# Optimization experiments

Measured on AMD Instinct MI355X. Metric: run time of the kernel, lower is better.

The kernel has to match this reference:

```python
import jax, jax.numpy as jnp
import numpy as np
import math

NUM_HEADS = 16


def rotate_half(x):
    # faithful to torch: take even/odd interleaved halves, cat(-x2, x1)
    x1 = x[..., ::2]
    x2 = x[..., 1::2]
    return jnp.concatenate((-x2, x1), axis=-1)


def rotary_tables(seq_len, head_dim, dtype):
    inv_freq = 1.0 / (10000.0 ** (jnp.arange(0, head_dim, 2, dtype=jnp.float32) / head_dim))
    t = jnp.arange(seq_len, dtype=jnp.float32)
    freqs = t[:, None] * inv_freq[None, :]           # [T, hd/2]
    emb = jnp.concatenate((freqs, freqs), axis=-1)   # [T, hd]
    cos = jnp.cos(emb)[None, None, :, :].astype(dtype)
    sin = jnp.sin(emb)[None, None, :, :].astype(dtype)
    return cos, sin


def setup_inputs() -> dict:
    key = jax.random.key(0)
    k1, k2, k3, k4 = jax.random.split(key, 4)
    B, T, D = 2, 2048, 1024
    scale = 1.0 / math.sqrt(D)
    x = jax.random.normal(k1, (B, T, D), dtype=jnp.float32)
    w_qkv = jax.random.normal(k2, (3 * D, D), dtype=jnp.float32) * scale
    w_out = jax.random.normal(k3, (D, D), dtype=jnp.float32) * scale
    b_out = jax.random.normal(k4, (D,), dtype=jnp.float32) * scale
    return {"x": x, "w_qkv": w_qkv, "w_out": w_out, "b_out": b_out}


def reference(x, w_qkv, w_out, b_out):
    B, T, D = x.shape
    H = NUM_HEADS
    hd = D // H

    qkv = x @ w_qkv.T                                # [B, T, 3D]
    q, k, v = jnp.split(qkv, 3, axis=-1)
    def to_heads(a):
        return a.reshape(B, T, H, hd).transpose(0, 2, 1, 3)  # [B, H, T, hd]
    q, k, v = to_heads(q), to_heads(k), to_heads(v)

    cos, sin = rotary_tables(T, hd, x.dtype)
    q = q * cos + rotate_half(q) * sin
    k = k * cos + rotate_half(k) * sin

    attn = jnp.einsum("bhqd,bhkd->bhqk", q, k) / math.sqrt(hd)
    attn = jax.nn.softmax(attn, axis=-1)
    out = jnp.einsum("bhqk,bhkd->bhqd", attn, v)
    out = out.transpose(0, 2, 1, 3).reshape(B, T, D)
    return out @ w_out.T + b_out
```

## Files before the change

kernel.cpp:

```cpp
#include <hip/hip_runtime.h>
#include <math.h>

#define B_ 2
#define T_ 2048
#define D_ 1024
#define H_ 16

typedef __attribute__((ext_vector_type(8))) short bf16x8;
typedef __attribute__((ext_vector_type(4))) float f32x4;
typedef __attribute__((address_space(3))) char lds_char;
typedef __attribute__((address_space(1))) const char g_char;

#define QSCALE 0.18033688011112042f
#define DEFER_THR 11.5f

static __device__ inline unsigned short bf16_rne(float f) {
    union { float f; unsigned u; } v; v.f = f;
    unsigned r = v.u + 0x7FFFu + ((v.u >> 16) & 1u);
    return (unsigned short)(r >> 16);
}
static __device__ inline unsigned pack2bf(float lo, float hi) {
    return (unsigned)bf16_rne(lo) | ((unsigned)bf16_rne(hi) << 16);
}

__global__ __launch_bounds__(256) void split_kernel(const float* __restrict__ in,
                                                    unsigned short* __restrict__ hi,
                                                    unsigned short* __restrict__ lo,
                                                    int n8) {
    int i = blockIdx.x * 256 + threadIdx.x;
    if (i >= n8) return;
    const float4* ip = (const float4*)in + (size_t)i * 2;
    float4 f0 = ip[0], f1 = ip[1];
    float fs[8] = {f0.x, f0.y, f0.z, f0.w, f1.x, f1.y, f1.z, f1.w};
    unsigned hu[4], lu[4];
#pragma unroll
    for (int j = 0; j < 4; ++j) {
        unsigned short h0 = bf16_rne(fs[2 * j]), h1 = bf16_rne(fs[2 * j + 1]);
        union { unsigned u; float f; } c0, c1;
        c0.u = (unsigned)h0 << 16; c1.u = (unsigned)h1 << 16;
        unsigned short l0 = bf16_rne(fs[2 * j] - c0.f);
        unsigned short l1 = bf16_rne(fs[2 * j + 1] - c1.f);
        hu[j] = (unsigned)h0 | ((unsigned)h1 << 16);
        lu[j] = (unsigned)l0 | ((unsigned)l1 << 16);
    }
    *(uint4*)(hi + (size_t)i * 8) = make_uint4(hu[0], hu[1], hu[2], hu[3]);
    *(uint4*)(lo + (size_t)i * 8) = make_uint4(lu[0], lu[1], lu[2], lu[3]);
}

__global__ __launch_bounds__(256) void rope_tables(float* __restrict__ cosT,
                                                   float* __restrict__ sinT) {
    int idx = blockIdx.x * 256 + threadIdx.x;
    int t = idx >> 5, i = idx & 31;
    double invf_d = exp(-((double)(2 * i) / 64.0) * 9.210340371976184);
    float invf = (float)invf_d;
    float ang = (float)t * invf;
    cosT[idx] = (float)cos((double)ang);
    sinT[idx] = (float)sin((double)ang);
}

template <int BIAS>
__global__ __launch_bounds__(256) void gemm_split(const unsigned short* __restrict__ Ahi,
                                                  const unsigned short* __restrict__ Alo,
                                                  const unsigned short* __restrict__ Bhi,
                                                  const unsigned short* __restrict__ Blo,
                                                  const float* __restrict__ bias,
                                                  float* __restrict__ C,
                                                  int M, int N, int K) {
    __shared__ alignas(16) char lds[32768];
    char* As_hi = lds;
    char* As_lo = lds + 8192;
    char* Bs_hi = lds + 16384;
    char* Bs_lo = lds + 24576;

    const int tid = threadIdx.x, l = tid & 63, w = tid >> 6;
    const int m0 = blockIdx.y * 128, n0 = blockIdx.x * 128;
    const int wr = (w >> 1) * 64, wc = (w & 1) * 64;
    const int q16 = l & 15, g8 = l >> 4;
    const int srow = w * 16 + (l >> 2);

    f32x4 acc[4][4];
#pragma unroll
    for (int i = 0; i < 4; ++i)
#pragma unroll
        for (int j = 0; j < 4; ++j) acc[i][j] = (f32x4){0.f, 0.f, 0.f, 0.f};

    for (int k0 = 0; k0 < K; k0 += 32) {
#pragma unroll
        for (int rd = 0; rd < 2; ++rd) {
            int row = srow + rd * 64;
            int g = (l & 3) ^ (row & 3);
            size_t goffA = (size_t)(m0 + row) * K + k0 + g * 8;
            size_t goffB = (size_t)(n0 + row) * K + k0 + g * 8;
            int lbase = rd * 4096 + w * 1024;
            __builtin_amdgcn_global_load_lds((g_char*)(Ahi + goffA), (lds_char*)(As_hi + lbase), 16, 0, 0);
            __builtin_amdgcn_global_load_lds((g_char*)(Alo + goffA), (lds_char*)(As_lo + lbase), 16, 0, 0);
            __builtin_amdgcn_global_load_lds((g_char*)(Bhi + goffB), (lds_char*)(Bs_hi + lbase), 16, 0, 0);
            __builtin_amdgcn_global_load_lds((g_char*)(Blo + goffB), (lds_char*)(Bs_lo + lbase), 16, 0, 0);
        }
        __syncthreads();

        bf16x8 ah[4], al[4], bh[4], bl[4];
#pragma unroll
        for (int i = 0; i < 4; ++i) {
            int ra = wr + 16 * i + q16, rb = wc + 16 * i + q16;
            ah[i] = *(const bf16x8*)(As_hi + ra * 64 + ((g8 ^ (ra & 3)) * 16));
            al[i] = *(const bf16x8*)(As_lo + ra * 64 + ((g8 ^ (ra & 3)) * 16));
            bh[i] = *(const bf16x8*)(Bs_hi + rb * 64 + ((g8 ^ (rb & 3)) * 16));
            bl[i] = *(const bf16x8*)(Bs_lo + rb * 64 + ((g8 ^ (rb & 3)) * 16));
        }
#pragma unroll
        for (int i = 0; i < 4; ++i)
#pragma unroll
            for (int j = 0; j < 4; ++j) {
                acc[i][j] = __builtin_amdgcn_mfma_f32_16x16x32_bf16(ah[i], bh[j], acc[i][j], 0, 0, 0);
                acc[i][j] = __builtin_amdgcn_mfma_f32_16x16x32_bf16(ah[i], bl[j], acc[i][j], 0, 0, 0);
                acc[i][j] = __builtin_amdgcn_mfma_f32_16x16x32_bf16(al[i], bh[j], acc[i][j], 0, 0, 0);
            }
        __syncthreads();
    }

#pragma unroll
    for (int i = 0; i < 4; ++i)
#pragma unroll
        for (int j = 0; j < 4; ++j) {
            int col = n0 + wc + 16 * j + q16;
            float badd = BIAS ? bias[col] : 0.f;
#pragma unroll
            for (int r = 0; r < 4; ++r) {
                int row = m0 + wr + 16 * i + 4 * g8 + r;
                C[(size_t)row * N + col] = acc[i][j][r] + badd;
            }
        }
}

__global__ __launch_bounds__(256) void prep_attn(const float* __restrict__ qkv,
                                                 const float* __restrict__ cosT,
                                                 const float* __restrict__ sinT,
                                                 unsigned short* __restrict__ qb,
                                                 unsigned short* __restrict__ kb,
                                                 unsigned short* __restrict__ vt) {
    __shared__ float vlds[64][65];
    const int tid = threadIdx.x;
    const int t0 = blockIdx.x * 64;
    const int bh = blockIdx.y;
    const int b = bh >> 4, h = bh & 15;

    if (tid < 128) {
        int sel = tid >> 6;
        int t = t0 + (tid & 63);
        const float* p = qkv + ((size_t)(b * T_ + t)) * 3072 + sel * 1024 + h * 64;
        float v[64];
#pragma unroll
        for (int d = 0; d < 64; d += 4) {
            float4 f = *reinterpret_cast<const float4*>(p + d);
            v[d] = f.x; v[d + 1] = f.y; v[d + 2] = f.z; v[d + 3] = f.w;
        }
        const float* c = cosT + t * 32;
        const float* s = sinT + t * 32;
        float o[64];
#pragma unroll
        for (int i = 0; i < 32; ++i) {
            float ci = c[i], si = s[i];
            o[i]      = v[i]      * ci - v[2 * i + 1] * si;
            o[i + 32] = v[i + 32] * ci + v[2 * i]     * si;
        }
        float sc = sel ? 1.0f : QSCALE;
        unsigned short* dst = (sel ? kb : qb) + ((size_t)bh * T_ + t) * 64;
#pragma unroll
        for (int d2 = 0; d2 < 8; ++d2) {
            uint4 u;
            u.x = pack2bf(o[8 * d2 + 0] * sc, o[8 * d2 + 1] * sc);
            u.y = pack2bf(o[8 * d2 + 2] * sc, o[8 * d2 + 3] * sc);
            u.z = pack2bf(o[8 * d2 + 4] * sc, o[8 * d2 + 5] * sc);
            u.w = pack2bf(o[8 * d2 + 6] * sc, o[8 * d2 + 7] * sc);
            *reinterpret_cast<uint4*>(dst + d2 * 8) = u;
        }
    } else {
        int tt = tid - 128;
        int row = tt >> 1, half = tt & 1;
        const float* p = qkv + ((size_t)(b * T_ + t0 + row)) * 3072 + 2048 + h * 64 + half * 32;
#pragma unroll
        for (int j = 0; j < 8; ++j) {
            float4 f = *reinterpret_cast<const float4*>(p + j * 4);
            vlds[row][half * 32 + j * 4 + 0] = f.x;
            vlds[row][half * 32 + j * 4 + 1] = f.y;
            vlds[row][half * 32 + j * 4 + 2] = f.z;
            vlds[row][half * 32 + j * 4 + 3] = f.w;
        }
    }
    __syncthreads();
    if (tid >= 128) {
        int tt = tid - 128;
        int d = tt >> 1, half = tt & 1;
        unsigned out[16];
#pragma unroll
        for (int j = 0; j < 16; ++j)
            out[j] = pack2bf(vlds[half * 32 + 2 * j][d], vlds[half * 32 + 2 * j + 1][d]);
        unsigned short* dst = vt + ((size_t)bh * 64 + d) * T_ + t0 + half * 32;
#pragma unroll
        for (int j = 0; j < 4; ++j)
            *reinterpret_cast<uint4*>(dst + j * 8) =
                make_uint4(out[4 * j], out[4 * j + 1], out[4 * j + 2], out[4 * j + 3]);
    }
}

static __device__ inline bf16x8 frag_read(const char* lds, int row, int elem0) {
    int byte = row * 128 + ((elem0 * 2) ^ ((row & 7) << 4));
    return *reinterpret_cast<const bf16x8*>(lds + byte);
}

static __device__ inline void stage_contig(const unsigned short* gtile, char* ldst,
                                           int w, int lane) {
#pragma unroll
    for (int n = 0; n < 2; ++n) {
        int loff = n * 4096 + w * 1024;
        int row = (loff >> 7) + (lane >> 3);
        int g = (lane & 7) ^ (row & 7);
        const unsigned short* src = gtile + row * 64 + g * 8;
        __builtin_amdgcn_global_load_lds((g_char*)src, (lds_char*)(ldst + loff), 16, 0, 0);
    }
}

static __device__ inline void stage_vt_tile(const unsigned short* vhead, int kt,
                                            char* ldst, int w, int lane) {
#pragma unroll
    for (int n = 0; n < 2; ++n) {
        int loff = n * 4096 + w * 1024;
        int row = (loff >> 7) + (lane >> 3);
        int g = (lane & 7) ^ (row & 7);
        const unsigned short* src = vhead + (size_t)row * T_ + kt * 64 + g * 8;
        __builtin_amdgcn_global_load_lds((g_char*)src, (lds_char*)(ldst + loff), 16, 0, 0);
    }
}

__global__ __launch_bounds__(256) void attn_mfma(const unsigned short* __restrict__ qb,
                                                 const unsigned short* __restrict__ kb,
                                                 const unsigned short* __restrict__ vt,
                                                 unsigned short* __restrict__ ctx_hi,
                                                 unsigned short* __restrict__ ctx_lo) {
    __shared__ alignas(16) char lds[40960];

    const int tid  = threadIdx.x;
    const int w    = tid >> 6;
    const int lane = tid & 63;
    const int g    = lane >> 4;
    const int q    = lane & 15;

    const int qbk = blockIdx.x;
    const int bh  = blockIdx.y;
    const int b   = bh >> 4, h = bh & 15;

    const unsigned short* qtile = qb + ((size_t)bh * T_ + qbk * 64) * 64;
    const unsigned short* khead = kb + (size_t)bh * T_ * 64;
    const unsigned short* vhead = vt + (size_t)bh * 64 * T_;

    stage_contig(qtile, lds, w, lane);
    stage_contig(khead, lds + 8192, w, lane);
    stage_vt_tile(vhead, 0, lds + 24576, w, lane);
    __syncthreads();

    const int qrow = 16 * w + q;
    bf16x8 bq0 = frag_read(lds, qrow, 8 * g);
    bf16x8 bq1 = frag_read(lds, qrow, 32 + 8 * g);

    f32x4 acc[4];
#pragma unroll
    for (int i = 0; i < 4; ++i) acc[i] = (f32x4){0.f, 0.f, 0.f, 0.f};
    float mrun = -INFINITY, lrun = 0.f;

    const int srcA = q + 32 * (g & 1);
    const int srcB = srcA + 16;
    const bool hiSel = (g >> 1) != 0;

    for (int kt = 0; kt < 32; ++kt) {
        const int cur = kt & 1;
        if (kt < 31) {
            stage_contig(khead + (size_t)(kt + 1) * 64 * 64, lds + 8192 + (cur ^ 1) * 8192, w, lane);
            stage_vt_tile(vhead, kt + 1, lds + 24576 + (cur ^ 1) * 8192, w, lane);
        }
        const char* kc = lds + 8192 + cur * 8192;
        const char* vc = lds + 24576 + cur * 8192;

        f32x4 st[4];
        __builtin_amdgcn_s_setprio(1);
#pragma unroll
        for (int mt = 0; mt < 4; ++mt) {
            int kvrow = 16 * mt + q;
            f32x4 c = (f32x4){0.f, 0.f, 0.f, 0.f};
            c = __builtin_amdgcn_mfma_f32_16x16x32_bf16(frag_read(kc, kvrow, 8 * g), bq0, c, 0, 0, 0);
            c = __builtin_amdgcn_mfma_f32_16x16x32_bf16(frag_read(kc, kvrow, 32 + 8 * g), bq1, c, 0, 0, 0);
            st[mt] = c;
        }
        __builtin_amdgcn_s_setprio(0);

        float tmax = st[0][0];
#pragma unroll
        for (int mt = 0; mt < 4; ++mt)
#pragma unroll
            for (int r = 0; r < 4; ++r) tmax = fmaxf(tmax, st[mt][r]);
        tmax = fmaxf(tmax, __shfl_xor(tmax, 16));
        tmax = fmaxf(tmax, __shfl_xor(tmax, 32));
        if (!__all(tmax - mrun <= DEFER_THR)) {
            float mnew = fmaxf(mrun, tmax);
            float corr = exp2f(mrun - mnew);
            lrun *= corr;
#pragma unroll
            for (int i = 0; i < 4; ++i) {
                acc[i][0] *= corr; acc[i][1] *= corr;
                acc[i][2] *= corr; acc[i][3] *= corr;
            }
            mrun = mnew;
        }
        float p[16];
        float tsum = 0.f;
#pragma unroll
        for (int mt = 0; mt < 4; ++mt)
#pragma unroll
            for (int r = 0; r < 4; ++r) {
                float e = exp2f(st[mt][r] - mrun);
                p[4 * mt + r] = e;
                tsum += e;
            }
        tsum += __shfl_xor(tsum, 16);
        tsum += __shfl_xor(tsum, 32);
        lrun += tsum;

        unsigned pk0[4], pk1[4];
#pragma unroll
        for (int mt = 0; mt < 4; ++mt) {
            pk0[mt] = pack2bf(p[4 * mt + 0], p[4 * mt + 1]);
            pk1[mt] = pack2bf(p[4 * mt + 2], p[4 * mt + 3]);
        }
        union { bf16x8 v; unsigned u[4]; } bp0, bp1;
        {
            unsigned xa0 = __shfl(pk0[0], srcA), ya0 = __shfl(pk0[1], srcA);
            unsigned xa1 = __shfl(pk1[0], srcA), ya1 = __shfl(pk1[1], srcA);
            unsigned xb0 = __shfl(pk0[0], srcB), yb0 = __shfl(pk0[1], srcB);
            unsigned xb1 = __shfl(pk1[0], srcB), yb1 = __shfl(pk1[1], srcB);
            bp0.u[0] = hiSel ? ya0 : xa0;
            bp0.u[1] = hiSel ? ya1 : xa1;
            bp0.u[2] = hiSel ? yb0 : xb0;
            bp0.u[3] = hiSel ? yb1 : xb1;
        }
        {
            unsigned xa0 = __shfl(pk0[2], srcA), ya0 = __shfl(pk0[3], srcA);
            unsigned xa1 = __shfl(pk1[2], srcA), ya1 = __shfl(pk1[3], srcA);
            unsigned xb0 = __shfl(pk0[2], srcB), yb0 = __shfl(pk0[3], srcB);
            unsigned xb1 = __shfl(pk1[2], srcB), yb1 = __shfl(pk1[3], srcB);
            bp1.u[0] = hiSel ? ya0 : xa0;
            bp1.u[1] = hiSel ? ya1 : xa1;
            bp1.u[2] = hiSel ? yb0 : xb0;
            bp1.u[3] = hiSel ? yb1 : xb1;
        }

        __builtin_amdgcn_s_setprio(1);
#pragma unroll
        for (int nt = 0; nt < 4; ++nt) {
            int nrow = 16 * nt + q;
            acc[nt] = __builtin_amdgcn_mfma_f32_16x16x32_bf16(frag_read(vc, nrow, 8 * g), bp0.v, acc[nt], 0, 0, 0);
            acc[nt] = __builtin_amdgcn_mfma_f32_16x16x32_bf16(frag_read(vc, nrow, 32 + 8 * g), bp1.v, acc[nt], 0, 0, 0);
        }
        __builtin_amdgcn_s_setprio(0);

        __syncthreads();
    }

    float inv_l = 1.0f / lrun;
    const int q_abs = qbk * 64 + 16 * w + q;
    size_t obase = ((size_t)b * T_ + q_abs) * 1024 + h * 64;
#pragma unroll
    for (int nt = 0; nt < 4; ++nt)
#pragma unroll
        for (int r = 0; r < 4; ++r) {
            float o = acc[nt][r] * inv_l;
            unsigned short hh = bf16_rne(o);
            union { unsigned u; float f; } hf; hf.u = (unsigned)hh << 16;
            unsigned short ll = bf16_rne(o - hf.f);
            ctx_hi[obase + 16 * nt + 4 * g + r] = hh;
            ctx_lo[obase + 16 * nt + 4 * g + r] = ll;
        }
}

extern "C" void kernel_launch(void* const* d_in, const int* in_sizes, int n_in,
                              void* d_out, int out_size, void* d_ws, size_t ws_size,
                              hipStream_t stream) {
    const float* x     = (const float*)d_in[0];
    const float* w_qkv = (const float*)d_in[1];
    const float* w_out = (const float*)d_in[2];
    const float* b_out = (const float*)d_in[3];
    float* out = (float*)d_out;

    char* base = (char*)d_ws;
    float* qkvF = (float*)base;
    unsigned short* x_hi = (unsigned short*)(base + 50331648);
    unsigned short* x_lo = (unsigned short*)(base + 58720256);
    unsigned short* wq_hi = (unsigned short*)(base + 67108864);
    unsigned short* wq_lo = (unsigned short*)(base + 73400320);
    unsigned short* qb16 = (unsigned short*)(base + 50331648);
    unsigned short* kb16 = (unsigned short*)(base + 58720256);
    unsigned short* vt16 = (unsigned short*)(base + 67108864);
    unsigned short* ctx_hi  = (unsigned short*)(base + 0);
    unsigned short* ctx_lo  = (unsigned short*)(base + 8388608);
    unsigned short* wout_hi = (unsigned short*)(base + 16777216);
    unsigned short* wout_lo = (unsigned short*)(base + 18874368);
    float* cosT = (float*)(base + 79691776);
    float* sinT = cosT + 65536;

    rope_tables<<<256, 256, 0, stream>>>(cosT, sinT);
    split_kernel<<<2048, 256, 0, stream>>>(x, x_hi, x_lo, 524288);
    split_kernel<<<1536, 256, 0, stream>>>(w_qkv, wq_hi, wq_lo, 393216);
    gemm_split<0><<<dim3(24, 32), 256, 0, stream>>>(x_hi, x_lo, wq_hi, wq_lo,
                                                    nullptr, qkvF, 4096, 3072, 1024);
    prep_attn<<<dim3(32, 32), 256, 0, stream>>>(qkvF, cosT, sinT, qb16, kb16, vt16);
    split_kernel<<<512, 256, 0, stream>>>(w_out, wout_hi, wout_lo, 131072);
    attn_mfma<<<dim3(32, 32), 256, 0, stream>>>(qb16, kb16, vt16, ctx_hi, ctx_lo);
    gemm_split<1><<<dim3(8, 32), 256, 0, stream>>>(ctx_hi, ctx_lo, wout_hi, wout_lo,
                                                   b_out, out, 4096, 1024, 1024);
}
```

Baseline: 324.8 us.

## Swizzle block order, use hardware exp2/bf16 pack, defer softmax row-sum reduction

Remaps block indices in the GEMM and attention kernels to an XCD-aware swizzle so that blocks sharing operands land on the same L2. In the attention inner loop, exp2f and the software bf16 rounding are replaced with raw v_exp_f32 and v_cvt_pk_bf16_f32 instructions. The per-tile cross-lane sum shuffles are removed by accumulating a per-lane partial sum and reducing it once at the end. The GEMM swizzle assumes the block count is divisible by 8, and raw v_exp_f32 skips the denormal handling that exp2f provides.

```diff
diff --git a/kernel.cpp b/kernel.cpp
--- a/kernel.cpp
+++ b/kernel.cpp
@@ -21,6 +21,12 @@
 }
 static __device__ inline unsigned pack2bf(float lo, float hi) {
     return (unsigned)bf16_rne(lo) | ((unsigned)bf16_rne(hi) << 16);
+}
+static __device__ inline float exp2_hw(float x) {
+    float r; asm("v_exp_f32 %0, %1" : "=v"(r) : "v"(x)); return r;
+}
+static __device__ inline unsigned cvt_pk_bf16(float lo, float hi) {
+    unsigned r; asm("v_cvt_pk_bf16_f32 %0, %1, %2" : "=v"(r) : "v"(lo), "v"(hi)); return r;
 }
 
 __global__ __launch_bounds__(256) void split_kernel(const float* __restrict__ in,
@@ -73,7 +79,12 @@
     char* Bs_lo = lds + 24576;
 
     const int tid = threadIdx.x, l = tid & 63, w = tid >> 6;
-    const int m0 = blockIdx.y * 128, n0 = blockIdx.x * 128;
+    const int nx = gridDim.x;
+    const int bid = blockIdx.y * nx + blockIdx.x;
+    const int cpx = (nx * gridDim.y) >> 3;
+    const int swz = (bid & 7) * cpx + (bid >> 3);
+    const int m0 = (swz / nx) * 128, n0 = (swz % nx) * 128;
+
     const int wr = (w >> 1) * 64, wc = (w & 1) * 64;
     const int q16 = l & 15, g8 = l >> 4;
     const int srow = w * 16 + (l >> 2);
@@ -246,8 +257,10 @@
     const int g    = lane >> 4;
     const int q    = lane & 15;
 
-    const int qbk = blockIdx.x;
-    const int bh  = blockIdx.y;
+    const int bid = blockIdx.y * 32 + blockIdx.x;
+    const int swz = (bid & 7) * 128 + (bid >> 3);
+    const int qbk = swz & 31;
+    const int bh  = swz >> 5;
     const int b   = bh >> 4, h = bh & 15;
 
     const unsigned short* qtile = qb + ((size_t)bh * T_ + qbk * 64) * 64;
@@ -266,7 +279,7 @@
     f32x4 acc[4];
 #pragma unroll
     for (int i = 0; i < 4; ++i) acc[i] = (f32x4){0.f, 0.f, 0.f, 0.f};
-    float mrun = -INFINITY, lrun = 0.f;
+    float mrun = -INFINITY, lsum = 0.f;
 
     const int srcA = q + 32 * (g & 1);
     const int srcB = srcA + 16;
@@ -293,17 +306,17 @@
         }
         __builtin_amdgcn_s_setprio(0);
 
-        float tmax = st[0][0];
-#pragma unroll
-        for (int mt = 0; mt < 4; ++mt)
-#pragma unroll
-            for (int r = 0; r < 4; ++r) tmax = fmaxf(tmax, st[mt][r]);
+        float tmax = fmaxf(fmaxf(st[0][0], st[0][1]), fmaxf(st[0][2], st[0][3]));
+#pragma unroll
+        for (int mt = 1; mt < 4; ++mt)
+            tmax = fmaxf(tmax, fmaxf(fmaxf(st[mt][0], st[mt][1]),
+                                     fmaxf(st[mt][2], st[mt][3])));
         tmax = fmaxf(tmax, __shfl_xor(tmax, 16));
         tmax = fmaxf(tmax, __shfl_xor(tmax, 32));
         if (!__all(tmax - mrun <= DEFER_THR)) {
             float mnew = fmaxf(mrun, tmax);
-            float corr = exp2f(mrun - mnew);
-            lrun *= corr;
+            float corr = exp2_hw(mrun - mnew);
+            lsum *= corr;
 #pragma unroll
             for (int i = 0; i < 4; ++i) {
                 acc[i][0] *= corr; acc[i][1] *= corr;
@@ -312,24 +325,20 @@
             mrun = mnew;
         }
         float p[16];
-        float tsum = 0.f;
 #pragma unroll
         for (int mt = 0; mt < 4; ++mt)
 #pragma unroll
             for (int r = 0; r < 4; ++r) {
-                float e = exp2f(st[mt][r] - mrun);
+                float e = exp2_hw(st[mt][r] - mrun);
                 p[4 * mt + r] = e;
-                tsum += e;
+                lsum += e;
             }
-        tsum += __shfl_xor(tsum, 16);
-        tsum += __shfl_xor(tsum, 32);
-        lrun += tsum;
 
         unsigned pk0[4], pk1[4];
 #pragma unroll
         for (int mt = 0; mt < 4; ++mt) {
-            pk0[mt] = pack2bf(p[4 * mt + 0], p[4 * mt + 1]);
-            pk1[mt] = pack2bf(p[4 * mt + 2], p[4 * mt + 3]);
+            pk0[mt] = cvt_pk_bf16(p[4 * mt + 0], p[4 * mt + 1]);
+            pk1[mt] = cvt_pk_bf16(p[4 * mt + 2], p[4 * mt + 3]);
         }
         union { bf16x8 v; unsigned u[4]; } bp0, bp1;
         {
@@ -365,7 +374,10 @@
         __syncthreads();
     }
 
-    float inv_l = 1.0f / lrun;
+    lsum += __shfl_xor(lsum, 16);
+    lsum += __shfl_xor(lsum, 32);
+
+    float inv_l = 1.0f / lsum;
     const int q_abs = qbk * 64 + 16 * w + q;
     size_t obase = ((size_t)b * T_ + q_abs) * 1024 + h * 64;
 #pragma unroll
```

After: 308.7 us. -4.9%, faster.
